# Kernel optimization log

Hardware: AMD Instinct MI355X
Metric: run time of the kernel (lower is better)

## Reference

```python
import jax, jax.numpy as jnp
import numpy as np

N_NODES = 50000
N_EDGES = 800000
IN_F = 128
OUT_F = 128
N_REL = 40
N_BASES = 30


def setup_inputs() -> dict:
    key = jax.random.key(0)
    k = jax.random.split(key, 8)
    x = jax.random.normal(k[0], (N_NODES, IN_F), dtype=jnp.float32)
    edge_index = jax.random.randint(k[1], (2, N_EDGES), 0, N_NODES, dtype=jnp.int64)
    edge_type = jax.random.randint(k[2], (N_EDGES,), 0, N_REL, dtype=jnp.int64)
    # Xavier-uniform-ish parameter init
    def xavier(kk, shape):
        fan_in, fan_out = shape[-2], shape[-1]
        a = float(np.sqrt(6.0 / (fan_in + fan_out)))
        return jax.random.uniform(kk, shape, jnp.float32, -a, a)
    weight = xavier(k[3], (N_BASES, IN_F, OUT_F))
    coeff = xavier(k[4], (N_REL, N_BASES))
    self_weight = xavier(k[5], (IN_F, OUT_F))
    bias = jnp.zeros((OUT_F,), dtype=jnp.float32)
    return {
        "x": x,
        "edge_index": edge_index,
        "edge_type": edge_type,
        "num_nodes": N_NODES,
        "weight": weight,
        "coeff": coeff,
        "self_weight": self_weight,
        "bias": bias,
    }


def reference(x, edge_index, edge_type, num_nodes, weight, coeff, self_weight, bias):
    # Basis decomposition: W_r = sum_b coeff[r,b] * V_b -> [R, in, out]
    rel_weight = jnp.einsum("rb,bio->rio", coeff, weight)
    # Since msg = x[src] @ W[r] == (x @ W[r])[src], transform all nodes for
    # all relations once, then gather per edge. h_all: [R, N, out]
    h_all = jnp.einsum("ni,rio->rno", x, rel_weight)
    src = edge_index[0]
    tgt = edge_index[1]
    msg = h_all[edge_type, src]  # [E, out]
    out = jax.ops.segment_sum(msg, tgt, num_segments=num_nodes)  # scatter-add
    # in-degree normalization, clamped at 1
    deg = jax.ops.segment_sum(jnp.ones_like(tgt, dtype=x.dtype), tgt,
                              num_segments=num_nodes)
    deg = jnp.maximum(deg, 1.0)
    out = out / deg[:, None]
    out = out + x @ self_weight  # self loop
    out = out + bias
    return out
```

## Files before the change

### kernel.cpp

```cpp
#include <hip/hip_runtime.h>

#define IN_F 128
#define OUT_F 128
#define MSG_GRID 2048

typedef unsigned int uint;
typedef unsigned short ushort;
typedef __attribute__((ext_vector_type(8))) short bf16x8;
typedef __attribute__((ext_vector_type(4))) float f32x4;
typedef __attribute__((ext_vector_type(4))) float f32x4e;
typedef __attribute__((ext_vector_type(2))) float f32x2e;
typedef __attribute__((ext_vector_type(4))) int i32x4;

typedef __attribute__((address_space(1))) void gvoid;
typedef __attribute__((address_space(3))) void svoid;

__device__ __forceinline__ void gl_lds16(const void* g, void* l) {
  __builtin_amdgcn_global_load_lds((const gvoid*)g, (svoid*)l, 16, 0, 0);
}

__device__ inline ushort f2bf(float f) {
  uint u = __float_as_uint(f);
  uint r = (u + 0x7FFFu + ((u >> 16) & 1u)) >> 16;
  return (ushort)r;
}

__global__ __launch_bounds__(256) void k_prep(
    const float* __restrict__ w, const float* __restrict__ coef,
    const float* __restrict__ selfw, ushort* __restrict__ rwT,
    const float* __restrict__ x, ushort* __restrict__ xbf, int n4,
    const int* __restrict__ etype, const int* __restrict__ tgt, int E, int R, int B,
    int* __restrict__ hist, int* __restrict__ ideg, int wblocks, int xblocks) {
  __shared__ float t[64][65];
  __shared__ int lh[64];
  int tid = threadIdx.x;
  int bid = blockIdx.x;

  if (bid < wblocks) {
    int r = bid >> 2;
    int i0 = (bid & 1) * 64;
    int o0 = ((bid >> 1) & 1) * 64;
    float4 a4[4];
    if (r < R) {
      #pragma unroll
      for (int it = 0; it < 4; ++it) a4[it] = make_float4(0.f, 0.f, 0.f, 0.f);
      for (int b = 0; b < B; ++b) {
        float cb = coef[r * B + b];
        const float4* w4 = (const float4*)w + (size_t)b * 4096;
        #pragma unroll
        for (int it = 0; it < 4; ++it) {
          int idx = it * 256 + tid;
          int i = idx >> 4, c4 = idx & 15;
          float4 v = w4[(i0 + i) * 32 + (o0 >> 2) + c4];
          a4[it].x = fmaf(cb, v.x, a4[it].x);
          a4[it].y = fmaf(cb, v.y, a4[it].y);
          a4[it].z = fmaf(cb, v.z, a4[it].z);
          a4[it].w = fmaf(cb, v.w, a4[it].w);
        }
      }
    } else {
      const float4* w4 = (const float4*)selfw;
      #pragma unroll
      for (int it = 0; it < 4; ++it) {
        int idx = it * 256 + tid;
        int i = idx >> 4, c4 = idx & 15;
        a4[it] = w4[(i0 + i) * 32 + (o0 >> 2) + c4];
      }
    }
    #pragma unroll
    for (int it = 0; it < 4; ++it) {
      int idx = it * 256 + tid;
      int i = idx >> 4, c4 = idx & 15;
      t[i][c4 * 4 + 0] = a4[it].x; t[i][c4 * 4 + 1] = a4[it].y;
      t[i][c4 * 4 + 2] = a4[it].z; t[i][c4 * 4 + 3] = a4[it].w;
    }
    __syncthreads();
    ushort* dst = rwT + (size_t)r * IN_F * OUT_F;
    #pragma unroll
    for (int it = 0; it < 4; ++it) {
      int idx = it * 256 + tid;
      int o = idx >> 4, cc = idx & 15;
      uint2 pk;
      pk.x = (uint)f2bf(t[cc * 4 + 0][o]) | ((uint)f2bf(t[cc * 4 + 1][o]) << 16);
      pk.y = (uint)f2bf(t[cc * 4 + 2][o]) | ((uint)f2bf(t[cc * 4 + 3][o]) << 16);
      *(uint2*)(dst + (o0 + o) * IN_F + i0 + cc * 4) = pk;
    }
    return;
  }
  bid -= wblocks;
  if (bid < xblocks) {
    int i = bid * 256 + tid;
    if (i < n4) {
      f32x4e v = __builtin_nontemporal_load((const f32x4e*)x + i);
      uint2 pk;
      pk.x = (uint)f2bf(v.x) | ((uint)f2bf(v.y) << 16);
      pk.y = (uint)f2bf(v.z) | ((uint)f2bf(v.w) << 16);
      ((uint2*)xbf)[i] = pk;
    }
    return;
  }
  bid -= xblocks;
  if (tid < R) lh[tid] = 0;
  __syncthreads();
  int e = bid * 256 + tid;
  if (e < E) {
    atomicAdd(&lh[etype[e]], 1);
    atomicAdd(&ideg[tgt[e]], 1);
  }
  __syncthreads();
  if (tid < R && lh[tid]) atomicAdd(&hist[tid], lh[tid]);
}

__global__ __launch_bounds__(1024) void k_scans(
    const int* __restrict__ hist, int* __restrict__ offs, int* __restrict__ toffs,
    int R, const int* __restrict__ ideg, int* __restrict__ row_off, int N) {
  __shared__ int part[1024];
  int tid = threadIdx.x;
  if (tid == 0) {
    int s = 0, tt = 0;
    for (int r = 0; r < R; ++r) {
      offs[r] = s; toffs[r] = tt;
      s += hist[r];
      tt += (hist[r] + 63) >> 6;
    }
    offs[R] = s; toffs[R] = tt;
  }
  int chunk = (((N + 1023) >> 10) + 3) & ~3;
  int lo = min(tid * chunk, N), hi = min(lo + chunk, N);
  int s = 0;
  int i = lo;
  for (; i + 4 <= hi; i += 4) {
    i32x4 v = *(const i32x4*)(ideg + i);
    s += v.x + v.y + v.z + v.w;
  }
  for (; i < hi; ++i) s += ideg[i];
  part[tid] = s;
  __syncthreads();
  for (int d = 1; d < 1024; d <<= 1) {
    int v = (tid >= d) ? part[tid - d] : 0;
    __syncthreads();
    part[tid] += v;
    __syncthreads();
  }
  int pre = (tid > 0) ? part[tid - 1] : 0;
  i = lo;
  for (; i + 4 <= hi; i += 4) {
    i32x4 v = *(const i32x4*)(ideg + i);
    i32x4 o;
    o.x = pre; o.y = pre + v.x; o.z = o.y + v.y; o.w = o.z + v.z;
    pre = o.w + v.w;
    *(i32x4*)(row_off + i) = o;
  }
  for (; i < hi; ++i) { row_off[i] = pre; pre += ideg[i]; }
  if (tid == 1023) row_off[N] = part[1023];
}

__global__ void k_scatter2(const int* __restrict__ etype, const int* __restrict__ src,
                           const int* __restrict__ tgt, int E, int R,
                           const int* __restrict__ offs, const int* __restrict__ row_off,
                           int* __restrict__ cur_r, int* __restrict__ cur_t,
                           int* __restrict__ perm, int* __restrict__ wpos) {
  __shared__ int lh[64], lbase[64], lcur[64];
  int tid = threadIdx.x;
  if (tid < R) { lh[tid] = 0; lcur[tid] = 0; }
  __syncthreads();
  int e = blockIdx.x * blockDim.x + tid;
  int t = -1;
  if (e < E) { t = etype[e]; atomicAdd(&lh[t], 1); }
  __syncthreads();
  if (tid < R) lbase[tid] = lh[tid] ? atomicAdd(&cur_r[tid], lh[tid]) : 0;
  __syncthreads();
  if (e < E) {
    int loc = atomicAdd(&lcur[t], 1);
    int slot = offs[t] + lbase[t] + loc;
    perm[slot] = src[e];
    int tg = tgt[e];
    int pos = row_off[tg] + atomicAdd(&cur_t[tg], 1);
    wpos[slot] = pos;
  }
}

__global__ __launch_bounds__(256) void k_msg(
    const ushort* __restrict__ xbf, const int* __restrict__ perm,
    const int* __restrict__ wpos, const int* __restrict__ offs,
    const int* __restrict__ toffs, const ushort* __restrict__ rwT,
    ushort* __restrict__ msg, int R) {
  __shared__ ushort xs[2][64 * IN_F];
  __shared__ int soff[48], stoff[48];
  int tid = threadIdx.x, wv = tid >> 6, l = tid & 63, g = l >> 4, ln = l & 15;
  int wc = wv * 32;
  int trow = tid >> 4, ts4 = tid & 15;

  if (tid <= R) { soff[tid] = offs[tid]; stoff[tid] = toffs[tid]; }
  __syncthreads();
  int ntiles = stoff[R];
  int chunkT = (ntiles + MSG_GRID - 1) / MSG_GRID;
  int t0 = blockIdx.x * chunkT;
  int tend = min(t0 + chunkT, ntiles);
  if (t0 >= tend) return;

  bf16x8 bfr[2][4];
#define LOADW(rr)                                                             \
  {                                                                           \
    const ushort* _wp = rwT + (size_t)(rr) * IN_F * OUT_F;                    \
    _Pragma("unroll")                                                         \
    for (int _n = 0; _n < 2; ++_n)                                            \
      _Pragma("unroll")                                                       \
      for (int _kk = 0; _kk < 4; ++_kk)                                       \
        bfr[_n][_kk] = *(const bf16x8*)(_wp + (wc + _n * 16 + ln) * IN_F +    \
                                        _kk * 32 + g * 8);                    \
  }

  int r0 = 0;
  while (t0 >= stoff[r0 + 1]) ++r0;

  bf16x8 xreg[4];
  int srcrow[4], wq[4];

  {
    int eb = soff[r0] + (t0 - stoff[r0]) * 64;
    int cnt = min(64, soff[r0 + 1] - eb);
    #pragma unroll
    for (int i = 0; i < 4; ++i) {
      int row = trow + 16 * i;
      int sr = perm[eb + min(row, cnt - 1)];
      xreg[i] = *(const bf16x8*)(xbf + (size_t)sr * IN_F + ts4 * 8);
    }
    #pragma unroll
    for (int i = 0; i < 4; ++i) {
      int row = trow + 16 * i;
      *(bf16x8*)((char*)xs[0] + row * 256 + ((ts4 * 16) ^ ((row & 7) << 4))) = xreg[i];
    }
    #pragma unroll
    for (int q = 0; q < 4; ++q) wq[q] = wpos[eb + min(q * 16 + ln, cnt - 1)];
  }
  if (t0 + 1 < tend) {
    int r1 = r0; while (t0 + 1 >= stoff[r1 + 1]) ++r1;
    int eb = soff[r1] + (t0 + 1 - stoff[r1]) * 64;
    int cnt = min(64, soff[r1 + 1] - eb);
    #pragma unroll
    for (int i = 0; i < 4; ++i) {
      int row = trow + 16 * i;
      int sr = perm[eb + min(row, cnt - 1)];
      xreg[i] = *(const bf16x8*)(xbf + (size_t)sr * IN_F + ts4 * 8);
    }
  }
  if (t0 + 2 < tend) {
    int r2 = r0; while (t0 + 2 >= stoff[r2 + 1]) ++r2;
    int eb = soff[r2] + (t0 + 2 - stoff[r2]) * 64;
    int cnt = min(64, soff[r2 + 1] - eb);
    #pragma unroll
    for (int i = 0; i < 4; ++i)
      srcrow[i] = perm[eb + min(trow + 16 * i, cnt - 1)];
  }
  LOADW(r0)
  int r_loaded = r0;
  int rcw = r0, rw1 = r0, rw3 = r0;
  int cur = 0;

  for (int t = t0; t < tend; ++t) {
    asm volatile("s_waitcnt lgkmcnt(0)" ::: "memory");
    __builtin_amdgcn_s_barrier();
    __builtin_amdgcn_sched_barrier(0);

    while (t >= stoff[rcw + 1]) ++rcw;
    int eb_t = soff[rcw] + (t - stoff[rcw]) * 64;
    int cnt_t = min(64, soff[rcw + 1] - eb_t);
    if (rcw != r_loaded) { LOADW(rcw) r_loaded = rcw; }

    const char* xb = (const char*)xs[cur];
    f32x4 acc[2][4] = {};
    #pragma unroll
    for (int kk = 0; kk < 4; ++kk) {
      bf16x8 a[4];
      #pragma unroll
      for (int q = 0; q < 4; ++q) {
        int row = q * 16 + ln;
        int kb = kk * 64 + g * 16;
        a[q] = *(const bf16x8*)(xb + row * 256 + (kb ^ ((row & 7) << 4)));
      }
      #pragma unroll
      for (int n = 0; n < 2; ++n)
        #pragma unroll
        for (int q = 0; q < 4; ++q)
          acc[n][q] = __builtin_amdgcn_mfma_f32_16x16x32_bf16(bfr[n][kk], a[q],
                                                              acc[n][q], 0, 0, 0);
    }

    #pragma unroll
    for (int q = 0; q < 4; ++q) {
      int rr = q * 16 + ln;
      if (rr < cnt_t) {
        ushort* mp = msg + (size_t)wq[q] * OUT_F + wc + g * 4;
        uint2 p0, p1;
        p0.x = (uint)f2bf(acc[0][q][0]) | ((uint)f2bf(acc[0][q][1]) << 16);
        p0.y = (uint)f2bf(acc[0][q][2]) | ((uint)f2bf(acc[0][q][3]) << 16);
        p1.x = (uint)f2bf(acc[1][q][0]) | ((uint)f2bf(acc[1][q][1]) << 16);
        p1.y = (uint)f2bf(acc[1][q][2]) | ((uint)f2bf(acc[1][q][3]) << 16);
        *(uint2*)mp = p0;
        *(uint2*)(mp + 16) = p1;
      }
    }

    if (t + 1 < tend) {
      char* xw = (char*)xs[cur ^ 1];
      #pragma unroll
      for (int i = 0; i < 4; ++i) {
        int row = trow + 16 * i;
        *(bf16x8*)(xw + row * 256 + ((ts4 * 16) ^ ((row & 7) << 4))) = xreg[i];
      }
    }

    if (t + 2 < tend) {
      #pragma unroll
      for (int i = 0; i < 4; ++i)
        xreg[i] = *(const bf16x8*)(xbf + (size_t)srcrow[i] * IN_F + ts4 * 8);
    }
    if (t + 3 < tend) {
      while (t + 3 >= stoff[rw3 + 1]) ++rw3;
      int eb = soff[rw3] + (t + 3 - stoff[rw3]) * 64;
      int cnt = min(64, soff[rw3 + 1] - eb);
      #pragma unroll
      for (int i = 0; i < 4; ++i)
        srcrow[i] = perm[eb + min(trow + 16 * i, cnt - 1)];
    }
    if (t + 1 < tend) {
      while (t + 1 >= stoff[rw1 + 1]) ++rw1;
      int eb = soff[rw1] + (t + 1 - stoff[rw1]) * 64;
      int cnt = min(64, soff[rw1 + 1] - eb);
      #pragma unroll
      for (int q = 0; q < 4; ++q) wq[q] = wpos[eb + min(q * 16 + ln, cnt - 1)];
    }
    cur ^= 1;
  }
#undef LOADW
}

__global__ __launch_bounds__(256) void k_out(
    const ushort* __restrict__ xbf, const ushort* __restrict__ swT,
    const float* __restrict__ bias, const ushort* __restrict__ msg,
    const int* __restrict__ row_off, float* __restrict__ out, int N) {
  __shared__ float smem[64 * 128];
  int tid = threadIdx.x;
  int base = blockIdx.x * 64;
  int wv = tid >> 6, l = tid & 63;
  char* xb = (char*)smem;

  #pragma unroll
  for (int i = 0; i < 4; ++i) {
    int idx = i * 256 + tid;
    int row = idx >> 4, s4 = idx & 15;
    int c = s4 ^ (row & 7);
    int n = base + row;
    char* lb = xb + i * 4096 + wv * 1024;
    if (n < N)
      gl_lds16(xbf + (size_t)n * IN_F + c * 8, lb);
  }

  int g = l >> 4, ln = l & 15, wc = wv * 32;
  bf16x8 bfr[2][4];
  #pragma unroll
  for (int n = 0; n < 2; ++n)
    #pragma unroll
    for (int kk = 0; kk < 4; ++kk)
      bfr[n][kk] = *(const bf16x8*)(swT + (wc + n * 16 + ln) * IN_F + kk * 32 + g * 8);

  __syncthreads();

  f32x4 acc[4][2] = {};
  #pragma unroll
  for (int kk = 0; kk < 4; ++kk) {
    bf16x8 a[4];
    #pragma unroll
    for (int m = 0; m < 4; ++m) {
      int row = m * 16 + ln;
      int kb = kk * 64 + g * 16;
      a[m] = *(const bf16x8*)(xb + row * 256 + (kb ^ ((row & 7) << 4)));
    }
    #pragma unroll
    for (int m = 0; m < 4; ++m)
      #pragma unroll
      for (int n = 0; n < 2; ++n)
        acc[m][n] = __builtin_amdgcn_mfma_f32_16x16x32_bf16(a[m], bfr[n][kk],
                                                            acc[m][n], 0, 0, 0);
  }

  __syncthreads();
  #pragma unroll
  for (int m = 0; m < 4; ++m)
    #pragma unroll
    for (int n = 0; n < 2; ++n)
      #pragma unroll
      for (int j = 0; j < 4; ++j)
        smem[(m * 16 + g * 4 + j) * 128 + wc + n * 16 + ln] = acc[m][n][j];
  __syncthreads();

  float b0 = bias[l * 2], b1 = bias[l * 2 + 1];
  for (int q = 0; q < 16; ++q) {
    int n = base + wv * 16 + q;
    if (n >= N) break;
    int lo = row_off[n], hi = row_off[n + 1];
    const uint* mp = (const uint*)msg + (size_t)lo * 64 + l;
    float a0 = 0.f, a1 = 0.f;
    int p = lo;
    for (; p + 8 <= hi; p += 8, mp += 512) {
      uint v0 = mp[0],   v1 = mp[64],  v2 = mp[128], v3 = mp[192];
      uint v4 = mp[256], v5 = mp[320], v6 = mp[384], v7 = mp[448];
      a0 += __uint_as_float(v0 << 16) + __uint_as_float(v1 << 16) +
            __uint_as_float(v2 << 16) + __uint_as_float(v3 << 16) +
            __uint_as_float(v4 << 16) + __uint_as_float(v5 << 16) +
            __uint_as_float(v6 << 16) + __uint_as_float(v7 << 16);
      a1 += __uint_as_float(v0 & 0xFFFF0000u) + __uint_as_float(v1 & 0xFFFF0000u) +
            __uint_as_float(v2 & 0xFFFF0000u) + __uint_as_float(v3 & 0xFFFF0000u) +
            __uint_as_float(v4 & 0xFFFF0000u) + __uint_as_float(v5 & 0xFFFF0000u) +
            __uint_as_float(v6 & 0xFFFF0000u) + __uint_as_float(v7 & 0xFFFF0000u);
    }
    for (; p + 2 <= hi; p += 2, mp += 128) {
      uint v0 = mp[0], v1 = mp[64];
      a0 += __uint_as_float(v0 << 16) + __uint_as_float(v1 << 16);
      a1 += __uint_as_float(v0 & 0xFFFF0000u) + __uint_as_float(v1 & 0xFFFF0000u);
    }
    for (; p < hi; ++p, mp += 64) {
      uint v = *mp;
      a0 += __uint_as_float(v << 16);
      a1 += __uint_as_float(v & 0xFFFF0000u);
    }
    float inv = 1.f / (float)max(hi - lo, 1);
    int rloc = wv * 16 + q;
    f32x2e o = {a0 * inv + smem[rloc * 128 + l * 2] + b0,
                a1 * inv + smem[rloc * 128 + l * 2 + 1] + b1};
    __builtin_nontemporal_store(o, (f32x2e*)(out + (size_t)n * OUT_F + l * 2));
  }
}

extern "C" void kernel_launch(void* const* d_in, const int* in_sizes, int n_in,
                              void* d_out, int out_size, void* d_ws, size_t ws_size,
                              hipStream_t stream) {
  const float* x      = (const float*)d_in[0];
  const int*   ei     = (const int*)d_in[1];
  const int*   etype  = (const int*)d_in[2];
  const float* weight = (const float*)d_in[4];
  const float* coeff  = (const float*)d_in[5];
  const float* selfw  = (const float*)d_in[6];
  const float* bias   = (const float*)d_in[7];

  int N = in_sizes[0] / IN_F;
  int E = in_sizes[2];
  int B = in_sizes[4] / (IN_F * OUT_F);
  int R = in_sizes[5] / B;
  const int* src = ei;
  const int* tgt = ei + E;

  char* ws = (char*)d_ws;
  size_t off = 0;
  auto alloc = [&](size_t bytes) {
    char* p = ws + off;
    off += (bytes + 255) & ~(size_t)255;
    return p;
  };
  ushort* rwT     = (ushort*)alloc((size_t)(R + 1) * IN_F * OUT_F * 2);
  ushort* xbf     = (ushort*)alloc((size_t)N * IN_F * 2);
  int*    perm    = (int*)alloc((size_t)E * 4);
  int*    wpos    = (int*)alloc((size_t)E * 4);
  int*    row_off = (int*)alloc((size_t)(N + 1) * 4);
  int*    ideg    = (int*)alloc((size_t)(2 * N + 128) * 4);
  int*    cur_t   = ideg + N;
  int*    hist    = cur_t + N;
  int*    cur_r   = hist + 64;
  int*    offs    = (int*)alloc(64 * 4);
  int*    toffs   = (int*)alloc(64 * 4);
  ushort* msg     = (ushort*)alloc((size_t)E * OUT_F * 2);

  (void)hipMemsetAsync(ideg, 0, (size_t)(2 * N + 128) * 4, stream);

  int n4 = N * IN_F / 4;
  int wblocks = (R + 1) * 4;
  int xblocks = (n4 + 255) / 256;
  int hblocks = (E + 255) / 256;
  k_prep<<<wblocks + xblocks + hblocks, 256, 0, stream>>>(
      weight, coeff, selfw, rwT, x, xbf, n4, etype, tgt, E, R, B,
      hist, ideg, wblocks, xblocks);
  k_scans<<<1, 1024, 0, stream>>>(hist, offs, toffs, R, ideg, row_off, N);
  k_scatter2<<<hblocks, 256, 0, stream>>>(etype, src, tgt, E, R, offs, row_off,
                                          cur_r, cur_t, perm, wpos);
  k_msg<<<MSG_GRID, 256, 0, stream>>>(xbf, perm, wpos, offs, toffs, rwT, msg, R);
  k_out<<<(N + 63) / 64, 256, 0, stream>>>(xbf, rwT + (size_t)R * IN_F * OUT_F,
                                           bias, msg, row_off, (float*)d_out, N);
}
```

Before: 294.5 us.

## Stage message tiles through LDS for full-row stores; widen segment-sum loads

In the message kernel, each tile's bf16 results are written to shared memory and then stored to global memory in the next iteration as full 16-byte row segments with nontemporal hints. Previously each lane scattered narrow 8-byte pieces. The gather prefetch is shortened from two tiles ahead to one, and an extra barrier is added per tile. In the output kernel, each wavefront now splits into two halves that read alternate message rows with 8-byte loads and combine the halves with a cross-lane shuffle, which cuts the number of load instructions. The cost is more barriers and shuffles, and less latency hiding on the gather.

Result: slower. 592.5 us (+101.2%).

```diff
diff --git a/kernel.cpp b/kernel.cpp
--- a/kernel.cpp
+++ b/kernel.cpp
@@ -11,6 +11,7 @@
 typedef __attribute__((ext_vector_type(4))) float f32x4e;
 typedef __attribute__((ext_vector_type(2))) float f32x2e;
 typedef __attribute__((ext_vector_type(4))) int i32x4;
+typedef __attribute__((ext_vector_type(2))) uint u32x2e;
 
 typedef __attribute__((address_space(1))) void gvoid;
 typedef __attribute__((address_space(3))) void svoid;
@@ -190,6 +191,7 @@
   int tid = threadIdx.x, wv = tid >> 6, l = tid & 63, g = l >> 4, ln = l & 15;
   int wc = wv * 32;
   int trow = tid >> 4, ts4 = tid & 15;
+  int srow = tid >> 2, sseg = tid & 3;
 
   if (tid <= R) { soff[tid] = offs[tid]; stoff[tid] = toffs[tid]; }
   __syncthreads();
@@ -211,19 +213,17 @@
                                         _kk * 32 + g * 8);                    \
   }
 
-  int r0 = 0;
-  while (t0 >= stoff[r0 + 1]) ++r0;
+  int rcw = 0;
+  while (t0 >= stoff[rcw + 1]) ++rcw;
+  int eb_t = soff[rcw] + (t0 - stoff[rcw]) * 64;
+  int cnt_t = min(64, soff[rcw + 1] - eb_t);
 
   bf16x8 xreg[4];
-  int srcrow[4], wq[4];
-
   {
-    int eb = soff[r0] + (t0 - stoff[r0]) * 64;
-    int cnt = min(64, soff[r0 + 1] - eb);
     #pragma unroll
     for (int i = 0; i < 4; ++i) {
       int row = trow + 16 * i;
-      int sr = perm[eb + min(row, cnt - 1)];
+      int sr = perm[eb_t + min(row, cnt_t - 1)];
       xreg[i] = *(const bf16x8*)(xbf + (size_t)sr * IN_F + ts4 * 8);
     }
     #pragma unroll
@@ -231,42 +231,42 @@
       int row = trow + 16 * i;
       *(bf16x8*)((char*)xs[0] + row * 256 + ((ts4 * 16) ^ ((row & 7) << 4))) = xreg[i];
     }
-    #pragma unroll
-    for (int q = 0; q < 4; ++q) wq[q] = wpos[eb + min(q * 16 + ln, cnt - 1)];
-  }
+  }
+  int rw2 = rcw;
+  int srcA[4] = {0, 0, 0, 0};
   if (t0 + 1 < tend) {
-    int r1 = r0; while (t0 + 1 >= stoff[r1 + 1]) ++r1;
+    int r1 = rcw; while (t0 + 1 >= stoff[r1 + 1]) ++r1;
     int eb = soff[r1] + (t0 + 1 - stoff[r1]) * 64;
     int cnt = min(64, soff[r1 + 1] - eb);
     #pragma unroll
-    for (int i = 0; i < 4; ++i) {
-      int row = trow + 16 * i;
-      int sr = perm[eb + min(row, cnt - 1)];
-      xreg[i] = *(const bf16x8*)(xbf + (size_t)sr * IN_F + ts4 * 8);
-    }
-  }
-  if (t0 + 2 < tend) {
-    int r2 = r0; while (t0 + 2 >= stoff[r2 + 1]) ++r2;
-    int eb = soff[r2] + (t0 + 2 - stoff[r2]) * 64;
-    int cnt = min(64, soff[r2 + 1] - eb);
-    #pragma unroll
-    for (int i = 0; i < 4; ++i)
-      srcrow[i] = perm[eb + min(trow + 16 * i, cnt - 1)];
-  }
-  LOADW(r0)
-  int r_loaded = r0;
-  int rcw = r0, rw1 = r0, rw3 = r0;
+    for (int i = 0; i < 4; ++i) srcA[i] = perm[eb + min(trow + 16 * i, cnt - 1)];
+  }
+  LOADW(rcw)
+  int r_loaded = rcw;
   int cur = 0;
+  int cnt_prev = 0, wprev = 0;
 
   for (int t = t0; t < tend; ++t) {
+    while (t >= stoff[rcw + 1]) ++rcw;
+    eb_t = soff[rcw] + (t - stoff[rcw]) * 64;
+    cnt_t = min(64, soff[rcw + 1] - eb_t);
+    if (rcw != r_loaded) { LOADW(rcw) r_loaded = rcw; }
+
     asm volatile("s_waitcnt lgkmcnt(0)" ::: "memory");
     __builtin_amdgcn_s_barrier();
     __builtin_amdgcn_sched_barrier(0);
 
-    while (t >= stoff[rcw + 1]) ++rcw;
-    int eb_t = soff[rcw] + (t - stoff[rcw]) * 64;
-    int cnt_t = min(64, soff[rcw + 1] - eb_t);
-    if (rcw != r_loaded) { LOADW(rcw) r_loaded = rcw; }
+    if (t > t0) {
+      const char* sb = (const char*)xs[cur ^ 1];
+      #pragma unroll
+      for (int k = 0; k < 4; ++k) {
+        bf16x8 sv = *(const bf16x8*)(sb + srow * 256 +
+                                     ((sseg * 64 + k * 16) ^ ((srow & 7) << 4)));
+        if (srow < cnt_prev)
+          __builtin_nontemporal_store(
+              sv, (bf16x8*)(msg + (size_t)wprev * OUT_F + sseg * 32 + k * 8));
+      }
+    }
 
     const char* xb = (const char*)xs[cur];
     f32x4 acc[2][4] = {};
@@ -287,21 +287,39 @@
                                                               acc[n][q], 0, 0, 0);
     }
 
-    #pragma unroll
-    for (int q = 0; q < 4; ++q) {
-      int rr = q * 16 + ln;
-      if (rr < cnt_t) {
-        ushort* mp = msg + (size_t)wq[q] * OUT_F + wc + g * 4;
-        uint2 p0, p1;
-        p0.x = (uint)f2bf(acc[0][q][0]) | ((uint)f2bf(acc[0][q][1]) << 16);
-        p0.y = (uint)f2bf(acc[0][q][2]) | ((uint)f2bf(acc[0][q][3]) << 16);
-        p1.x = (uint)f2bf(acc[1][q][0]) | ((uint)f2bf(acc[1][q][1]) << 16);
-        p1.y = (uint)f2bf(acc[1][q][2]) | ((uint)f2bf(acc[1][q][3]) << 16);
-        *(uint2*)mp = p0;
-        *(uint2*)(mp + 16) = p1;
-      }
-    }
-
+    int wstore = wpos[eb_t + min(srow, cnt_t - 1)];
+    if (t + 1 < tend) {
+      #pragma unroll
+      for (int i = 0; i < 4; ++i)
+        xreg[i] = *(const bf16x8*)(xbf + (size_t)srcA[i] * IN_F + ts4 * 8);
+    }
+    int srcB[4] = {srcA[0], srcA[1], srcA[2], srcA[3]};
+    if (t + 2 < tend) {
+      while (t + 2 >= stoff[rw2 + 1]) ++rw2;
+      int eb2 = soff[rw2] + (t + 2 - stoff[rw2]) * 64;
+      int cnt2 = min(64, soff[rw2 + 1] - eb2);
+      #pragma unroll
+      for (int i = 0; i < 4; ++i) srcB[i] = perm[eb2 + min(trow + 16 * i, cnt2 - 1)];
+    }
+
+    asm volatile("s_waitcnt lgkmcnt(0)" ::: "memory");
+    __builtin_amdgcn_s_barrier();
+    __builtin_amdgcn_sched_barrier(0);
+
+    {
+      char* st = (char*)xs[cur];
+      #pragma unroll
+      for (int q = 0; q < 4; ++q)
+        #pragma unroll
+        for (int n = 0; n < 2; ++n) {
+          int row = q * 16 + ln;
+          int colb = wv * 64 + n * 32 + g * 8;
+          uint2 pk;
+          pk.x = (uint)f2bf(acc[n][q][0]) | ((uint)f2bf(acc[n][q][1]) << 16);
+          pk.y = (uint)f2bf(acc[n][q][2]) | ((uint)f2bf(acc[n][q][3]) << 16);
+          *(uint2*)(st + row * 256 + (colb ^ ((row & 7) << 4))) = pk;
+        }
+    }
     if (t + 1 < tend) {
       char* xw = (char*)xs[cur ^ 1];
       #pragma unroll
@@ -311,27 +329,26 @@
       }
     }
 
-    if (t + 2 < tend) {
-      #pragma unroll
-      for (int i = 0; i < 4; ++i)
-        xreg[i] = *(const bf16x8*)(xbf + (size_t)srcrow[i] * IN_F + ts4 * 8);
-    }
-    if (t + 3 < tend) {
-      while (t + 3 >= stoff[rw3 + 1]) ++rw3;
-      int eb = soff[rw3] + (t + 3 - stoff[rw3]) * 64;
-      int cnt = min(64, soff[rw3 + 1] - eb);
-      #pragma unroll
-      for (int i = 0; i < 4; ++i)
-        srcrow[i] = perm[eb + min(trow + 16 * i, cnt - 1)];
-    }
-    if (t + 1 < tend) {
-      while (t + 1 >= stoff[rw1 + 1]) ++rw1;
-      int eb = soff[rw1] + (t + 1 - stoff[rw1]) * 64;
-      int cnt = min(64, soff[rw1 + 1] - eb);
-      #pragma unroll
-      for (int q = 0; q < 4; ++q) wq[q] = wpos[eb + min(q * 16 + ln, cnt - 1)];
-    }
+    cnt_prev = cnt_t;
+    wprev = wstore;
+    #pragma unroll
+    for (int i = 0; i < 4; ++i) srcA[i] = srcB[i];
     cur ^= 1;
+  }
+
+  asm volatile("s_waitcnt lgkmcnt(0)" ::: "memory");
+  __builtin_amdgcn_s_barrier();
+  __builtin_amdgcn_sched_barrier(0);
+  {
+    const char* sb = (const char*)xs[cur ^ 1];
+    #pragma unroll
+    for (int k = 0; k < 4; ++k) {
+      bf16x8 sv = *(const bf16x8*)(sb + srow * 256 +
+                                   ((sseg * 64 + k * 16) ^ ((srow & 7) << 4)));
+      if (srow < cnt_prev)
+        __builtin_nontemporal_store(
+            sv, (bf16x8*)(msg + (size_t)wprev * OUT_F + sseg * 32 + k * 8));
+    }
   }
 #undef LOADW
 }
@@ -395,41 +412,49 @@
         smem[(m * 16 + g * 4 + j) * 128 + wc + n * 16 + ln] = acc[m][n][j];
   __syncthreads();
 
-  float b0 = bias[l * 2], b1 = bias[l * 2 + 1];
+  int half = l >> 5, cl = l & 31;
+  f32x4e b4 = ((const f32x4e*)bias)[cl];
   for (int q = 0; q < 16; ++q) {
     int n = base + wv * 16 + q;
     if (n >= N) break;
     int lo = row_off[n], hi = row_off[n + 1];
-    const uint* mp = (const uint*)msg + (size_t)lo * 64 + l;
-    float a0 = 0.f, a1 = 0.f;
-    int p = lo;
-    for (; p + 8 <= hi; p += 8, mp += 512) {
-      uint v0 = mp[0],   v1 = mp[64],  v2 = mp[128], v3 = mp[192];
-      uint v4 = mp[256], v5 = mp[320], v6 = mp[384], v7 = mp[448];
-      a0 += __uint_as_float(v0 << 16) + __uint_as_float(v1 << 16) +
-            __uint_as_float(v2 << 16) + __uint_as_float(v3 << 16) +
-            __uint_as_float(v4 << 16) + __uint_as_float(v5 << 16) +
-            __uint_as_float(v6 << 16) + __uint_as_float(v7 << 16);
-      a1 += __uint_as_float(v0 & 0xFFFF0000u) + __uint_as_float(v1 & 0xFFFF0000u) +
-            __uint_as_float(v2 & 0xFFFF0000u) + __uint_as_float(v3 & 0xFFFF0000u) +
-            __uint_as_float(v4 & 0xFFFF0000u) + __uint_as_float(v5 & 0xFFFF0000u) +
-            __uint_as_float(v6 & 0xFFFF0000u) + __uint_as_float(v7 & 0xFFFF0000u);
-    }
-    for (; p + 2 <= hi; p += 2, mp += 128) {
-      uint v0 = mp[0], v1 = mp[64];
-      a0 += __uint_as_float(v0 << 16) + __uint_as_float(v1 << 16);
-      a1 += __uint_as_float(v0 & 0xFFFF0000u) + __uint_as_float(v1 & 0xFFFF0000u);
-    }
-    for (; p < hi; ++p, mp += 64) {
-      uint v = *mp;
-      a0 += __uint_as_float(v << 16);
-      a1 += __uint_as_float(v & 0xFFFF0000u);
-    }
-    float inv = 1.f / (float)max(hi - lo, 1);
-    int rloc = wv * 16 + q;
-    f32x2e o = {a0 * inv + smem[rloc * 128 + l * 2] + b0,
-                a1 * inv + smem[rloc * 128 + l * 2 + 1] + b1};
-    __builtin_nontemporal_store(o, (f32x2e*)(out + (size_t)n * OUT_F + l * 2));
+    int len = hi - lo;
+    const ushort* mrow = msg + (size_t)(lo + half) * OUT_F + cl * 4;
+    float fa0 = 0.f, fa1 = 0.f, fa2 = 0.f, fa3 = 0.f;
+#define ACC8(v)                                                  \
+    { fa0 += __uint_as_float((v).x << 16);                       \
+      fa1 += __uint_as_float((v).x & 0xFFFF0000u);               \
+      fa2 += __uint_as_float((v).y << 16);                       \
+      fa3 += __uint_as_float((v).y & 0xFFFF0000u); }
+    int p = 0;
+    for (; p + 8 <= len; p += 8) {
+      u32x2e v0 = __builtin_nontemporal_load((const u32x2e*)(mrow + (size_t)p * OUT_F));
+      u32x2e v1 = __builtin_nontemporal_load((const u32x2e*)(mrow + (size_t)(p + 2) * OUT_F));
+      u32x2e v2 = __builtin_nontemporal_load((const u32x2e*)(mrow + (size_t)(p + 4) * OUT_F));
+      u32x2e v3 = __builtin_nontemporal_load((const u32x2e*)(mrow + (size_t)(p + 6) * OUT_F));
+      ACC8(v0) ACC8(v1) ACC8(v2) ACC8(v3)
+    }
+    for (; p + 2 <= len; p += 2) {
+      u32x2e v = __builtin_nontemporal_load((const u32x2e*)(mrow + (size_t)p * OUT_F));
+      ACC8(v)
+    }
+    if (p < len && half == 0) {
+      u32x2e v = __builtin_nontemporal_load((const u32x2e*)(mrow + (size_t)p * OUT_F));
+      ACC8(v)
+    }
+#undef ACC8
+    fa0 += __shfl_xor(fa0, 32);
+    fa1 += __shfl_xor(fa1, 32);
+    fa2 += __shfl_xor(fa2, 32);
+    fa3 += __shfl_xor(fa3, 32);
+    if (half == 0) {
+      float inv = 1.f / (float)max(len, 1);
+      int rloc = wv * 16 + q;
+      f32x4e s4 = *(const f32x4e*)(&smem[rloc * 128 + cl * 4]);
+      f32x4e o = {fa0 * inv + s4.x + b4.x, fa1 * inv + s4.y + b4.y,
+                  fa2 * inv + s4.z + b4.z, fa3 * inv + s4.w + b4.w};
+      __builtin_nontemporal_store(o, (f32x4e*)(out + (size_t)n * OUT_F + cl * 4));
+    }
   }
 }
 
```
